# Kernel optimization log

Measured on AMD Instinct MI355X. Metric: run time of the kernel, lower is better.

The kernel has to match this reference:

```python
import jax, jax.numpy as jnp
import numpy as np

N_NODES = 50000


def _gcn_conv(x, src, dst, W, b, n):
    # PyG GCNConv: linear transform, add self-loops, symmetric norm, scatter-sum, bias.
    h = x @ W  # [N, out]
    loop = jnp.arange(n, dtype=src.dtype)
    s = jnp.concatenate([src, loop])
    d = jnp.concatenate([dst, loop])
    deg = jax.ops.segment_sum(jnp.ones_like(d, dtype=h.dtype), d, num_segments=n)
    dinv = jax.lax.rsqrt(jnp.maximum(deg, 1.0))  # deg >= 1 thanks to self-loops
    norm = dinv[s] * dinv[d]  # [E+N]
    msg = h[s] * norm[:, None]
    out = jax.ops.segment_sum(msg, d, num_segments=n)
    return out + b


def setup_inputs() -> dict:
    key = jax.random.key(0)
    ks = jax.random.split(key, 8)
    N, E = N_NODES, 800000
    d_in, d_hid, d_out = 128, 64, 128
    x = jax.random.normal(ks[0], (N, d_in), dtype=jnp.float32)
    edge_index = jax.random.randint(ks[1], (2, E), 0, N, dtype=jnp.int64)
    s = 1.0 / np.sqrt(d_in)
    W1 = jax.random.normal(ks[2], (d_in, d_hid), dtype=jnp.float32) * s
    b1 = jnp.zeros((d_hid,), dtype=jnp.float32)
    Wl = jax.random.normal(ks[3], (d_hid, d_out), dtype=jnp.float32) * (1.0 / np.sqrt(d_hid))
    bl = jnp.zeros((d_out,), dtype=jnp.float32)
    W2 = jax.random.normal(ks[4], (d_hid, d_out), dtype=jnp.float32) * (1.0 / np.sqrt(d_hid))
    b2 = jnp.zeros((d_out,), dtype=jnp.float32)
    return {"x": x, "edge_index": edge_index, "W1": W1, "b1": b1,
            "Wl": Wl, "bl": bl, "W2": W2, "b2": b2}


def reference(x, edge_index, W1, b1, Wl, bl, W2, b2):
    n = x.shape[0]
    src, dst = edge_index[0], edge_index[1]
    h = _gcn_conv(x, src, dst, W1, b1, n)          # conv1 -> [N, 64]
    x1 = h @ Wl + bl                               # residual linear branch [N, 128]
    h = jax.nn.relu(h)
    out = _gcn_conv(h, src, dst, W2, b2, n)        # conv2 -> [N, 128]
    return out + x + x1
```

## Files before the change

kernel.cpp:

```cpp
#include <hip/hip_runtime.h>
#include <hip/hip_fp16.h>

#define DIN 128
#define DH 64
#define DOUT 128
#define STRIDE 64

__global__ __launch_bounds__(256) void k_fill(const int* __restrict__ src,
                                              const int* __restrict__ dst,
                                              int* __restrict__ cnt,
                                              unsigned short* __restrict__ csr, int E) {
  int e = blockIdx.x * 256 + threadIdx.x;
  if (e < E) {
    int d = dst[e];
    int slot = atomicAdd(&cnt[d], 1);
    if (slot < STRIDE) csr[(long)d * STRIDE + slot] = (unsigned short)src[e];
  }
}

__global__ __launch_bounds__(256) void k_gemm1(const float* __restrict__ x,
                                               const float* __restrict__ W1,
                                               __half* __restrict__ h0,
                                               const int* __restrict__ cnt,
                                               float* __restrict__ dinv, int n) {
  const int t = threadIdx.x;
  for (int i = blockIdx.x * 256 + t; i < n; i += gridDim.x * 256)
    dinv[i] = rsqrtf(1.0f + (float)min(cnt[i], STRIDE));

  __shared__ float Ws[DIN * DH];
  __shared__ float xs[32][DIN + 4];
  for (int i = t; i < DIN * DH; i += 256) Ws[i] = W1[i];
  const int row0 = blockIdx.x * 32;
  for (int i = t; i < 32 * (DIN / 4); i += 256) {
    int r = i >> 5;
    int k4 = (i & 31) * 4;
    float4 v = make_float4(0.f, 0.f, 0.f, 0.f);
    int row = row0 + r;
    if (row < n) v = *(const float4*)&x[(long)row * DIN + k4];
    *(float4*)&xs[r][k4] = v;
  }
  __syncthreads();
  const int tc = t & 15, tr = t >> 4;
  const int col4 = tc * 4, r0 = tr * 2;
  float acc[2][4];
#pragma unroll
  for (int r = 0; r < 2; r++)
#pragma unroll
    for (int c = 0; c < 4; c++) acc[r][c] = 0.f;
  for (int k4 = 0; k4 < DIN; k4 += 4) {
    float4 xv[2];
#pragma unroll
    for (int r = 0; r < 2; r++) xv[r] = *(const float4*)&xs[r0 + r][k4];
#pragma unroll
    for (int kk = 0; kk < 4; kk++) {
      float4 wv = *(const float4*)&Ws[(k4 + kk) * DH + col4];
#pragma unroll
      for (int r = 0; r < 2; r++) {
        float xval = (&xv[r].x)[kk];
        acc[r][0] = fmaf(xval, wv.x, acc[r][0]);
        acc[r][1] = fmaf(xval, wv.y, acc[r][1]);
        acc[r][2] = fmaf(xval, wv.z, acc[r][2]);
        acc[r][3] = fmaf(xval, wv.w, acc[r][3]);
      }
    }
  }
#pragma unroll
  for (int r = 0; r < 2; r++) {
    int row = row0 + r0 + r;
    if (row < n) {
      union { uint2 u; __half2 h[2]; } sv;
      sv.h[0] = __floats2half2_rn(acc[r][0], acc[r][1]);
      sv.h[1] = __floats2half2_rn(acc[r][2], acc[r][3]);
      *(uint2*)&h0[(long)row * DH + col4] = sv.u;
    }
  }
}

__global__ __launch_bounds__(256) void k_gather1(const int* __restrict__ cnt,
                                                 const unsigned short* __restrict__ csr,
                                                 const float* __restrict__ dinv,
                                                 const __half* __restrict__ h0,
                                                 const float* __restrict__ b1,
                                                 float* __restrict__ h1,
                                                 __half* __restrict__ r16, int n) {
  long gid = (long)blockIdx.x * 256 + threadIdx.x;
  int node = (int)(gid >> 3);
  if (node >= n) return;
  int l = (int)(gid & 7);
  const float dd = dinv[node];
  const int deg = min(cnt[node], STRIDE);
  const long base = (long)node * STRIDE;
  float acc[8];
#pragma unroll
  for (int k = 0; k < 8; k++) acc[k] = 0.f;

  auto edge = [&](int s) {
    float w = dinv[s] * dd;
    union { uint4 u; __half2 h[4]; } c;
    c.u = *(const uint4*)&h0[(long)s * DH + l * 8];
#pragma unroll
    for (int k = 0; k < 4; k++) {
      float2 f = __half22float2(c.h[k]);
      acc[2 * k] = fmaf(f.x, w, acc[2 * k]);
      acc[2 * k + 1] = fmaf(f.y, w, acc[2 * k + 1]);
    }
  };

  int j = 0;
  for (; j + 4 <= deg; j += 4) {
    ushort4 cs = *(const ushort4*)&csr[base + j];
    edge(cs.x); edge(cs.y); edge(cs.z); edge(cs.w);
  }
  for (; j < deg; j++) edge(csr[base + j]);

  const float w = dd * dd;
  union { uint4 u; __half2 h[4]; } cs;
  cs.u = *(const uint4*)&h0[(long)node * DH + l * 8];
  float4 ba = *(const float4*)&b1[l * 8];
  float4 bb = *(const float4*)&b1[l * 8 + 4];
  float o[8];
#pragma unroll
  for (int k = 0; k < 4; k++) {
    float2 f = __half22float2(cs.h[k]);
    o[2 * k] = f.x * w + acc[2 * k];
    o[2 * k + 1] = f.y * w + acc[2 * k + 1];
  }
  o[0] += ba.x; o[1] += ba.y; o[2] += ba.z; o[3] += ba.w;
  o[4] += bb.x; o[5] += bb.y; o[6] += bb.z; o[7] += bb.w;
  *(float4*)&h1[(long)node * DH + l * 8] = make_float4(o[0], o[1], o[2], o[3]);
  *(float4*)&h1[(long)node * DH + l * 8 + 4] = make_float4(o[4], o[5], o[6], o[7]);
  union { uint4 u; __half2 h[4]; } rv;
#pragma unroll
  for (int k = 0; k < 4; k++)
    rv.h[k] = __floats2half2_rn(fmaxf(o[2 * k], 0.f), fmaxf(o[2 * k + 1], 0.f));
  *(uint4*)&r16[(long)node * DH + l * 8] = rv.u;
}

__global__ __launch_bounds__(256) void k_gather2C(const int* __restrict__ cnt,
                                                  const unsigned short* __restrict__ csr,
                                                  const float* __restrict__ dinv,
                                                  const __half* __restrict__ r16,
                                                  const float* __restrict__ h1,
                                                  const float* __restrict__ Wl,
                                                  const float* __restrict__ W2,
                                                  const float* __restrict__ bl,
                                                  const float* __restrict__ b2,
                                                  const float* __restrict__ x,
                                                  float* __restrict__ out, int n) {
  __shared__ float hs[32][DH + 4];
  const int t = threadIdx.x;
  const int row0 = blockIdx.x * 32;

  {
    const int r = t >> 3;
    const int l = t & 7;
    int node = row0 + r;
    float acc[8];
#pragma unroll
    for (int k = 0; k < 8; k++) acc[k] = 0.f;
    if (node < n) {
      const float dd = dinv[node];
      const int deg = min(cnt[node], STRIDE);
      const long base = (long)node * STRIDE;
      auto edge = [&](int s) {
        float w = dinv[s] * dd;
        union { uint4 u; __half2 h[4]; } c;
        c.u = *(const uint4*)&r16[(long)s * DH + l * 8];
#pragma unroll
        for (int k = 0; k < 4; k++) {
          float2 f = __half22float2(c.h[k]);
          acc[2 * k] = fmaf(f.x, w, acc[2 * k]);
          acc[2 * k + 1] = fmaf(f.y, w, acc[2 * k + 1]);
        }
      };
      int j = 0;
      for (; j + 4 <= deg; j += 4) {
        ushort4 cs = *(const ushort4*)&csr[base + j];
        edge(cs.x); edge(cs.y); edge(cs.z); edge(cs.w);
      }
      for (; j < deg; j++) edge(csr[base + j]);
      const float w = dd * dd;
      union { uint4 u; __half2 h[4]; } cs;
      cs.u = *(const uint4*)&r16[(long)node * DH + l * 8];
#pragma unroll
      for (int k = 0; k < 4; k++) {
        float2 f = __half22float2(cs.h[k]);
        acc[2 * k] = fmaf(f.x, w, acc[2 * k]);
        acc[2 * k + 1] = fmaf(f.y, w, acc[2 * k + 1]);
      }
    }
    *(float4*)&hs[r][l * 8] = make_float4(acc[0], acc[1], acc[2], acc[3]);
    *(float4*)&hs[r][l * 8 + 4] = make_float4(acc[4], acc[5], acc[6], acc[7]);
  }

  const int tc = t & 31, tr = t >> 5;
  const int col4 = tc * 4, r0 = tr * 4;
  float acc[4][4];
#pragma unroll
  for (int r = 0; r < 4; r++)
#pragma unroll
    for (int c = 0; c < 4; c++) acc[r][c] = 0.f;

  __syncthreads();
  for (int k4 = 0; k4 < DH; k4 += 4) {
    float4 hv[4];
#pragma unroll
    for (int r = 0; r < 4; r++) hv[r] = *(const float4*)&hs[r0 + r][k4];
#pragma unroll
    for (int kk = 0; kk < 4; kk++) {
      float4 wv = *(const float4*)&W2[(k4 + kk) * DOUT + col4];
#pragma unroll
      for (int r = 0; r < 4; r++) {
        float hval = (&hv[r].x)[kk];
        acc[r][0] = fmaf(hval, wv.x, acc[r][0]);
        acc[r][1] = fmaf(hval, wv.y, acc[r][1]);
        acc[r][2] = fmaf(hval, wv.z, acc[r][2]);
        acc[r][3] = fmaf(hval, wv.w, acc[r][3]);
      }
    }
  }
  __syncthreads();

  for (int i = t; i < 32 * (DH / 4); i += 256) {
    int r = i >> 4;
    int k4 = (i & 15) * 4;
    float4 v = make_float4(0.f, 0.f, 0.f, 0.f);
    int row = row0 + r;
    if (row < n) v = *(const float4*)&h1[(long)row * DH + k4];
    *(float4*)&hs[r][k4] = v;
  }
  __syncthreads();
  for (int k4 = 0; k4 < DH; k4 += 4) {
    float4 hv[4];
#pragma unroll
    for (int r = 0; r < 4; r++) hv[r] = *(const float4*)&hs[r0 + r][k4];
#pragma unroll
    for (int kk = 0; kk < 4; kk++) {
      float4 wv = *(const float4*)&Wl[(k4 + kk) * DOUT + col4];
#pragma unroll
      for (int r = 0; r < 4; r++) {
        float hval = (&hv[r].x)[kk];
        acc[r][0] = fmaf(hval, wv.x, acc[r][0]);
        acc[r][1] = fmaf(hval, wv.y, acc[r][1]);
        acc[r][2] = fmaf(hval, wv.z, acc[r][2]);
        acc[r][3] = fmaf(hval, wv.w, acc[r][3]);
      }
    }
  }

  float4 blv = *(const float4*)&bl[col4];
  float4 b2v = *(const float4*)&b2[col4];
#pragma unroll
  for (int r = 0; r < 4; r++) {
    int row = row0 + r0 + r;
    if (row < n) {
      float4 xv = *(const float4*)&x[(long)row * DOUT + col4];
      float4 o;
      o.x = xv.x + acc[r][0] + blv.x + b2v.x;
      o.y = xv.y + acc[r][1] + blv.y + b2v.y;
      o.z = xv.z + acc[r][2] + blv.z + b2v.z;
      o.w = xv.w + acc[r][3] + blv.w + b2v.w;
      *(float4*)&out[(long)row * DOUT + col4] = o;
    }
  }
}

extern "C" void kernel_launch(void* const* d_in, const int* in_sizes, int n_in,
                              void* d_out, int out_size, void* d_ws, size_t ws_size,
                              hipStream_t stream) {
  const float* x = (const float*)d_in[0];
  const int* edge_index = (const int*)d_in[1];
  const float* W1 = (const float*)d_in[2];
  const float* b1 = (const float*)d_in[3];
  const float* Wl = (const float*)d_in[4];
  const float* bl = (const float*)d_in[5];
  const float* W2 = (const float*)d_in[6];
  const float* b2 = (const float*)d_in[7];
  float* out = (float*)d_out;

  const int n = in_sizes[0] / DIN;
  const int E = in_sizes[1] / 2;
  const int* src = edge_index;
  const int* dst = edge_index + E;

  char* p = (char*)d_ws;
  auto alloc = [&](size_t bytes) { char* r = p; p += (bytes + 255) & ~(size_t)255; return r; };
  int* cnt = (int*)alloc((size_t)n * 4);
  unsigned short* csr = (unsigned short*)alloc((size_t)n * STRIDE * 2);
  float* dinv = (float*)alloc((size_t)n * 4);
  __half* h0 = (__half*)alloc((size_t)n * DH * 2);
  __half* r16 = (__half*)alloc((size_t)n * DH * 2);
  float* h1 = (float*)alloc((size_t)n * DH * 4);

  const int B = 256;
  hipMemsetAsync(cnt, 0, (size_t)n * sizeof(int), stream);
  k_fill<<<(E + B - 1) / B, B, 0, stream>>>(src, dst, cnt, csr, E);
  k_gemm1<<<(n + 31) / 32, B, 0, stream>>>(x, W1, h0, cnt, dinv, n);
  k_gather1<<<(int)(((long)n * 8 + B - 1) / B), B, 0, stream>>>(cnt, csr, dinv, h0, b1, h1, r16, n);
  k_gather2C<<<(n + 31) / 32, B, 0, stream>>>(cnt, csr, dinv, r16, h1, Wl, W2, bl, b2, x, out, n);
}
```

Measured before the change: 211.8 us.

## Batch 8 gathered loads per iteration and merge dual GEMMs in gather2 epilogue

Both gather kernels now read 8 CSR indices at once and issue all 8 neighbour-row loads and dinv loads before any FMAs, so more memory requests are in flight per thread. In gather2 the h1 tile is prefetched into registers before the gather and stored to a second shared buffer. The two sequential small GEMMs (W2 and Wl) become one fused loop, which removes two barriers and one reload pass. The cost is higher register pressure from the 8-deep load arrays and double the shared memory per block, which could lower occupancy.

```diff
diff --git a/kernel.cpp b/kernel.cpp
--- a/kernel.cpp
+++ b/kernel.cpp
@@ -94,24 +94,45 @@
 #pragma unroll
   for (int k = 0; k < 8; k++) acc[k] = 0.f;
 
-  auto edge = [&](int s) {
+  int j = 0;
+  for (; j + 8 <= deg; j += 8) {
+    uint4 iv = *(const uint4*)&csr[base + j];
+    int s[8];
+    s[0] = iv.x & 0xffff; s[1] = iv.x >> 16;
+    s[2] = iv.y & 0xffff; s[3] = iv.y >> 16;
+    s[4] = iv.z & 0xffff; s[5] = iv.z >> 16;
+    s[6] = iv.w & 0xffff; s[7] = iv.w >> 16;
+    uint4 c[8];
+    float w[8];
+#pragma unroll
+    for (int k = 0; k < 8; k++) {
+      c[k] = *(const uint4*)&h0[(long)s[k] * DH + l * 8];
+      w[k] = dinv[s[k]];
+    }
+#pragma unroll
+    for (int k = 0; k < 8; k++) {
+      float wk = w[k] * dd;
+      union { uint4 u; __half2 h[4]; } cc; cc.u = c[k];
+#pragma unroll
+      for (int q = 0; q < 4; q++) {
+        float2 f = __half22float2(cc.h[q]);
+        acc[2 * q] = fmaf(f.x, wk, acc[2 * q]);
+        acc[2 * q + 1] = fmaf(f.y, wk, acc[2 * q + 1]);
+      }
+    }
+  }
+  for (; j < deg; j++) {
+    int s = csr[base + j];
     float w = dinv[s] * dd;
     union { uint4 u; __half2 h[4]; } c;
     c.u = *(const uint4*)&h0[(long)s * DH + l * 8];
 #pragma unroll
-    for (int k = 0; k < 4; k++) {
-      float2 f = __half22float2(c.h[k]);
-      acc[2 * k] = fmaf(f.x, w, acc[2 * k]);
-      acc[2 * k + 1] = fmaf(f.y, w, acc[2 * k + 1]);
-    }
-  };
-
-  int j = 0;
-  for (; j + 4 <= deg; j += 4) {
-    ushort4 cs = *(const ushort4*)&csr[base + j];
-    edge(cs.x); edge(cs.y); edge(cs.z); edge(cs.w);
-  }
-  for (; j < deg; j++) edge(csr[base + j]);
+    for (int q = 0; q < 4; q++) {
+      float2 f = __half22float2(c.h[q]);
+      acc[2 * q] = fmaf(f.x, w, acc[2 * q]);
+      acc[2 * q + 1] = fmaf(f.y, w, acc[2 * q + 1]);
+    }
+  }
 
   const float w = dd * dd;
   union { uint4 u; __half2 h[4]; } cs;
@@ -147,9 +168,19 @@
                                                   const float* __restrict__ b2,
                                                   const float* __restrict__ x,
                                                   float* __restrict__ out, int n) {
-  __shared__ float hs[32][DH + 4];
+  __shared__ float hz[32][DH + 4];
+  __shared__ float hh[32][DH + 4];
   const int t = threadIdx.x;
   const int row0 = blockIdx.x * 32;
+
+  float4 p0 = make_float4(0.f, 0.f, 0.f, 0.f), p1 = p0;
+  {
+    int i0 = t, i1 = t + 256;
+    int ra = i0 >> 4, ca = (i0 & 15) * 4;
+    int rb = i1 >> 4, cb = (i1 & 15) * 4;
+    if (row0 + ra < n) p0 = *(const float4*)&h1[(long)(row0 + ra) * DH + ca];
+    if (row0 + rb < n) p1 = *(const float4*)&h1[(long)(row0 + rb) * DH + cb];
+  }
 
   {
     const int r = t >> 3;
@@ -162,23 +193,45 @@
       const float dd = dinv[node];
       const int deg = min(cnt[node], STRIDE);
       const long base = (long)node * STRIDE;
-      auto edge = [&](int s) {
+      int j = 0;
+      for (; j + 8 <= deg; j += 8) {
+        uint4 iv = *(const uint4*)&csr[base + j];
+        int s[8];
+        s[0] = iv.x & 0xffff; s[1] = iv.x >> 16;
+        s[2] = iv.y & 0xffff; s[3] = iv.y >> 16;
+        s[4] = iv.z & 0xffff; s[5] = iv.z >> 16;
+        s[6] = iv.w & 0xffff; s[7] = iv.w >> 16;
+        uint4 c[8];
+        float w[8];
+#pragma unroll
+        for (int k = 0; k < 8; k++) {
+          c[k] = *(const uint4*)&r16[(long)s[k] * DH + l * 8];
+          w[k] = dinv[s[k]];
+        }
+#pragma unroll
+        for (int k = 0; k < 8; k++) {
+          float wk = w[k] * dd;
+          union { uint4 u; __half2 h[4]; } cc; cc.u = c[k];
+#pragma unroll
+          for (int q = 0; q < 4; q++) {
+            float2 f = __half22float2(cc.h[q]);
+            acc[2 * q] = fmaf(f.x, wk, acc[2 * q]);
+            acc[2 * q + 1] = fmaf(f.y, wk, acc[2 * q + 1]);
+          }
+        }
+      }
+      for (; j < deg; j++) {
+        int s = csr[base + j];
         float w = dinv[s] * dd;
         union { uint4 u; __half2 h[4]; } c;
         c.u = *(const uint4*)&r16[(long)s * DH + l * 8];
 #pragma unroll
-        for (int k = 0; k < 4; k++) {
-          float2 f = __half22float2(c.h[k]);
-          acc[2 * k] = fmaf(f.x, w, acc[2 * k]);
-          acc[2 * k + 1] = fmaf(f.y, w, acc[2 * k + 1]);
+        for (int q = 0; q < 4; q++) {
+          float2 f = __half22float2(c.h[q]);
+          acc[2 * q] = fmaf(f.x, w, acc[2 * q]);
+          acc[2 * q + 1] = fmaf(f.y, w, acc[2 * q + 1]);
         }
-      };
-      int j = 0;
-      for (; j + 4 <= deg; j += 4) {
-        ushort4 cs = *(const ushort4*)&csr[base + j];
-        edge(cs.x); edge(cs.y); edge(cs.z); edge(cs.w);
-      }
-      for (; j < deg; j++) edge(csr[base + j]);
+      }
       const float w = dd * dd;
       union { uint4 u; __half2 h[4]; } cs;
       cs.u = *(const uint4*)&r16[(long)node * DH + l * 8];
@@ -189,9 +242,16 @@
         acc[2 * k + 1] = fmaf(f.y, w, acc[2 * k + 1]);
       }
     }
-    *(float4*)&hs[r][l * 8] = make_float4(acc[0], acc[1], acc[2], acc[3]);
-    *(float4*)&hs[r][l * 8 + 4] = make_float4(acc[4], acc[5], acc[6], acc[7]);
-  }
+    *(float4*)&hz[r][l * 8] = make_float4(acc[0], acc[1], acc[2], acc[3]);
+    *(float4*)&hz[r][l * 8 + 4] = make_float4(acc[4], acc[5], acc[6], acc[7]);
+  }
+
+  {
+    int i0 = t, i1 = t + 256;
+    *(float4*)&hh[i0 >> 4][(i0 & 15) * 4] = p0;
+    *(float4*)&hh[i1 >> 4][(i1 & 15) * 4] = p1;
+  }
+  __syncthreads();
 
   const int tc = t & 31, tr = t >> 5;
   const int col4 = tc * 4, r0 = tr * 4;
@@ -200,50 +260,25 @@
   for (int r = 0; r < 4; r++)
 #pragma unroll
     for (int c = 0; c < 4; c++) acc[r][c] = 0.f;
-
-  __syncthreads();
   for (int k4 = 0; k4 < DH; k4 += 4) {
-    float4 hv[4];
-#pragma unroll
-    for (int r = 0; r < 4; r++) hv[r] = *(const float4*)&hs[r0 + r][k4];
+    float4 zv[4], hv[4];
+#pragma unroll
+    for (int r = 0; r < 4; r++) {
+      zv[r] = *(const float4*)&hz[r0 + r][k4];
+      hv[r] = *(const float4*)&hh[r0 + r][k4];
+    }
 #pragma unroll
     for (int kk = 0; kk < 4; kk++) {
-      float4 wv = *(const float4*)&W2[(k4 + kk) * DOUT + col4];
+      float4 w2v = *(const float4*)&W2[(k4 + kk) * DOUT + col4];
+      float4 wlv = *(const float4*)&Wl[(k4 + kk) * DOUT + col4];
 #pragma unroll
       for (int r = 0; r < 4; r++) {
+        float zval = (&zv[r].x)[kk];
         float hval = (&hv[r].x)[kk];
-        acc[r][0] = fmaf(hval, wv.x, acc[r][0]);
-        acc[r][1] = fmaf(hval, wv.y, acc[r][1]);
-        acc[r][2] = fmaf(hval, wv.z, acc[r][2]);
-        acc[r][3] = fmaf(hval, wv.w, acc[r][3]);
-      }
-    }
-  }
-  __syncthreads();
-
-  for (int i = t; i < 32 * (DH / 4); i += 256) {
-    int r = i >> 4;
-    int k4 = (i & 15) * 4;
-    float4 v = make_float4(0.f, 0.f, 0.f, 0.f);
-    int row = row0 + r;
-    if (row < n) v = *(const float4*)&h1[(long)row * DH + k4];
-    *(float4*)&hs[r][k4] = v;
-  }
-  __syncthreads();
-  for (int k4 = 0; k4 < DH; k4 += 4) {
-    float4 hv[4];
-#pragma unroll
-    for (int r = 0; r < 4; r++) hv[r] = *(const float4*)&hs[r0 + r][k4];
-#pragma unroll
-    for (int kk = 0; kk < 4; kk++) {
-      float4 wv = *(const float4*)&Wl[(k4 + kk) * DOUT + col4];
-#pragma unroll
-      for (int r = 0; r < 4; r++) {
-        float hval = (&hv[r].x)[kk];
-        acc[r][0] = fmaf(hval, wv.x, acc[r][0]);
-        acc[r][1] = fmaf(hval, wv.y, acc[r][1]);
-        acc[r][2] = fmaf(hval, wv.z, acc[r][2]);
-        acc[r][3] = fmaf(hval, wv.w, acc[r][3]);
+        acc[r][0] = fmaf(zval, w2v.x, fmaf(hval, wlv.x, acc[r][0]));
+        acc[r][1] = fmaf(zval, w2v.y, fmaf(hval, wlv.y, acc[r][1]));
+        acc[r][2] = fmaf(zval, w2v.z, fmaf(hval, wlv.z, acc[r][2]));
+        acc[r][3] = fmaf(zval, w2v.w, fmaf(hval, wlv.w, acc[r][3]));
       }
     }
   }
```

Result: slower. 223.7 us (+5.6%).
